# Kernel optimization log

Measured on AMD Instinct MI355X. Metric: run time of the kernel, lower is better.

## Reference

```python
import jax, jax.numpy as jnp
import numpy as np

FP8_MAX = 448.0  # finfo(float8_e4m3fn).max
G = 128          # quantization block size


def _fp8_roundtrip(x):
    # emulate storage/rounding in float8_e4m3fn
    return x.astype(jnp.float8_e4m3fn).astype(jnp.float32)


def _quant_dequant_act(x, g=G):
    """Dynamic per-token, per-128-column-group fp8 quantization, then dequant.
    Matches fp8_act_quant: scale = amax(group)/FP8_MAX, q = clip(x/scale)."""
    lead, K = x.shape[:-1], x.shape[-1]
    xg = x.reshape(*lead, K // g, g)
    amax = jnp.max(jnp.abs(xg), axis=-1, keepdims=True)
    scale = jnp.maximum(amax, 1e-10) / FP8_MAX
    q = _fp8_roundtrip(jnp.clip(xg / scale, -FP8_MAX, FP8_MAX))
    return (q * scale).reshape(*lead, K)


def _dequant_weight(w, s, g=G):
    """Block-wise dequant: w [E,O,K] fp8 codes (stored as f32), s [E,O/g,K/g] scales."""
    E, O, K = w.shape
    wb = w.reshape(E, O // g, g, K // g, g)
    return (wb * s[:, :, None, :, None]).reshape(E, O, K)


def setup_inputs() -> dict:
    key = jax.random.key(0)
    ks = jax.random.split(key, 7)
    T, H, I, E, TK = 2048, 1024, 512, 16, 4
    hidden_states = jax.random.normal(ks[0], (T, H), dtype=jnp.float32)
    top_k_index = jax.random.randint(ks[1], (T, TK), 0, E)
    top_k_weights = jax.nn.softmax(jax.random.normal(ks[2], (T, TK), dtype=jnp.float32), axis=-1)
    # fp8-representable weight codes + positive block scale grids
    gate_up_proj = _fp8_roundtrip(jax.random.normal(ks[3], (E, 2 * I, H), dtype=jnp.float32) * 8.0)
    gate_up_proj_scale_inv = jax.random.uniform(ks[4], (E, (2 * I) // G, H // G), dtype=jnp.float32,
                                                minval=0.001, maxval=0.005)
    down_proj = _fp8_roundtrip(jax.random.normal(ks[5], (E, H, I), dtype=jnp.float32) * 8.0)
    down_proj_scale_inv = jax.random.uniform(ks[6], (E, H // G, I // G), dtype=jnp.float32,
                                             minval=0.001, maxval=0.005)
    return {
        "hidden_states": hidden_states,
        "top_k_index": top_k_index,
        "top_k_weights": top_k_weights,
        "gate_up_proj": gate_up_proj,
        "gate_up_proj_scale_inv": gate_up_proj_scale_inv,
        "down_proj": down_proj,
        "down_proj_scale_inv": down_proj_scale_inv,
    }


def reference(hidden_states, top_k_index, top_k_weights,
              gate_up_proj, gate_up_proj_scale_inv,
              down_proj, down_proj_scale_inv):
    E = gate_up_proj.shape[0]
    # dynamic activation quant (identical for every expert, since tokens are just gathered rows)
    x_deq = _quant_dequant_act(hidden_states)                       # [T, H]
    w_gu = _dequant_weight(gate_up_proj, gate_up_proj_scale_inv)    # [E, 2I, H]
    w_dn = _dequant_weight(down_proj, down_proj_scale_inv)          # [E, H, I]
    # gate_up GEMM for all experts; tokens not routed to e contribute with weight 0 below
    gate_up = jnp.einsum('th,eoh->teo', x_deq, w_gu)                # [T, E, 2I]
    gate, up = jnp.split(gate_up, 2, axis=-1)
    h = jax.nn.silu(gate) * up                                      # [T, E, I]
    h_deq = _quant_dequant_act(h)                                   # re-quantize intermediate
    expert_out = jnp.einsum('tei,ehi->teh', h_deq, w_dn)            # [T, E, H]
    # routing weight per (token, expert): sum of top_k weights whose index == e
    rw = jnp.einsum('tk,tke->te', top_k_weights,
                    jax.nn.one_hot(top_k_index, E, dtype=hidden_states.dtype))
    return jnp.einsum('teh,te->th', expert_out, rw)                 # [T, H] float32 accumulation
```

## Files before the change

### kernel.cpp

```cpp
#include <hip/hip_runtime.h>
#include <math.h>

#define T_TOK 2048
#define H_DIM 1024
#define I_DIM 512
#define N_EXP 16
#define TOPK  4
#define NPAIR (T_TOK*TOPK)

typedef unsigned short u16;
typedef unsigned char u8;
typedef __attribute__((ext_vector_type(4))) float f4v;

#define GLDS(g, l) __builtin_amdgcn_global_load_lds( \
    (const __attribute__((address_space(1))) void*)(g), \
    (__attribute__((address_space(3))) void*)(l), 16, 0, 0)

__device__ __forceinline__ float fp8_rt(float v) {
    float av = fabsf(v);
    if (av < 0.015625f) {
        return rintf(v * 512.0f) * 0.001953125f;
    }
    unsigned u = __float_as_uint(v);
    unsigned lsb = (u >> 20) & 1u;
    u = (u + 0x7FFFFu + lsb) & 0xFFF00000u;
    return __uint_as_float(u);
}

__device__ __forceinline__ unsigned f2fp8(float v) {
    unsigned u = __float_as_uint(v);
    unsigned s = (u >> 24) & 0x80u;
    float av = fabsf(v);
    if (av < 0.015625f) return s | (unsigned)(av * 512.0f);
    unsigned e = ((u >> 23) & 0xFFu) - 120u;
    return s | (e << 3) | ((u >> 20) & 7u);
}

__global__ void k_route2(const int* __restrict__ tki, int* __restrict__ counts,
                         int* __restrict__ lists) {
    __shared__ int cnt[16];
    int tid = threadIdx.x;
    if (tid < 16) cnt[tid] = 0;
    __syncthreads();
    #pragma unroll
    for (int j = 0; j < 8; ++j) {
        int p = tid * 8 + j;
        int e = tki[p];
        int pos = atomicAdd(&cnt[e], 1);
        lists[e * NPAIR + pos] = p;
    }
    __syncthreads();
    if (tid < 16) counts[tid] = cnt[tid];
}

#define NF4_GU (N_EXP * 2 * I_DIM * H_DIM / 4)
__global__ void k_prep(const float* __restrict__ wgu, u8* __restrict__ wgu_f8,
                       const float* __restrict__ wdn, u8* __restrict__ wdn_f8,
                       const float* __restrict__ x, u8* __restrict__ xq,
                       float* __restrict__ xs) {
    int bid = blockIdx.x, tid = threadIdx.x;
    if (bid < 24576) {
        int i = bid * 256 + tid;
        const float* in = wgu; u8* out = wgu_f8;
        if (i >= NF4_GU) { in = wdn; out = wdn_f8; i -= NF4_GU; }
        float4 a = ((const float4*)in)[i];
        unsigned pk = f2fp8(a.x) | (f2fp8(a.y) << 8) | (f2fp8(a.z) << 16) | (f2fp8(a.w) << 24);
        ((unsigned*)out)[i] = pk;
    } else {
        int t = bid - 24576;
        float4 v = ((const float4*)(x + (size_t)t * H_DIM))[tid];
        float a = fmaxf(fmaxf(fabsf(v.x), fabsf(v.y)), fmaxf(fabsf(v.z), fabsf(v.w)));
        #pragma unroll
        for (int m = 16; m >= 1; m >>= 1) a = fmaxf(a, __shfl_xor(a, m));
        float s = fmaxf(a, 1e-10f) / 448.0f;
        unsigned pk = f2fp8(fp8_rt(fminf(fmaxf(v.x / s, -448.f), 448.f)))
                    | (f2fp8(fp8_rt(fminf(fmaxf(v.y / s, -448.f), 448.f))) << 8)
                    | (f2fp8(fp8_rt(fminf(fmaxf(v.z / s, -448.f), 448.f))) << 16)
                    | (f2fp8(fp8_rt(fminf(fmaxf(v.w / s, -448.f), 448.f))) << 24);
        ((unsigned*)(xq + (size_t)t * H_DIM))[tid] = pk;
        if ((tid & 31) == 0) xs[t * 8 + (tid >> 5)] = s;
    }
}

__global__ __launch_bounds__(256, 3)
void k_gateup(const u8* __restrict__ xq, const float* __restrict__ xs,
              const int* __restrict__ counts, const int* __restrict__ lists,
              const u8* __restrict__ wgu, const float* __restrict__ sgu,
              const u8* __restrict__ zbuf, float* __restrict__ hbuf) {
    int bid = blockIdx.x;
    int e = bid & 15, tile = bid >> 4;
    int tt = tile >> 3, it = tile & 7;
    int n = counts[e];
    if (tt * 64 >= n) return;

    __shared__ __align__(16) u8 sm[2][24576];
    __shared__ float xs_l[64][8];
    __shared__ int ptok[64];

    int tid = threadIdx.x;
    int w = tid >> 6, lane = tid & 63;
    int m = w & 1, q = w >> 1;
    int l15 = lane & 15, l4 = lane >> 4;

    if (tid < 64) {
        int slot = tt * 64 + tid;
        ptok[tid] = (slot < n) ? lists[e * NPAIR + slot] : -1;
    }
    __syncthreads();
    {
        int r = tid >> 2, kb4 = (tid & 3) * 2;
        int p = ptok[r];
        xs_l[r][kb4]     = (p >= 0) ? xs[(p >> 2) * 8 + kb4]     : 0.f;
        xs_l[r][kb4 + 1] = (p >= 0) ? xs[(p >> 2) * 8 + kb4 + 1] : 0.f;
    }

    const u8* wbase = wgu + (size_t)e * (2 * I_DIM) * H_DIM;
    const u8* srcB[4];
    #pragma unroll
    for (int j = 0; j < 4; ++j) {
        int s = j * 256 + tid;
        int row = s >> 3, c8 = s & 7, cg = c8 ^ (row & 7);
        int nrow = (row < 64) ? it * 64 + row : 448 + it * 64 + row;
        srcB[j] = wbase + (size_t)nrow * H_DIM + cg * 16;
    }
    const u8* srcA[2];
    #pragma unroll
    for (int j = 0; j < 2; ++j) {
        int s = j * 256 + tid;
        int row = s >> 3, c8 = s & 7, cg = c8 ^ (row & 7);
        int p = ptok[row];
        srcA[j] = (p >= 0) ? xq + (size_t)(p >> 2) * H_DIM + cg * 16 : zbuf;
    }

    int idxA[2][4], idxB[4][4];
    #pragma unroll
    for (int fm = 0; fm < 2; ++fm) {
        int ar = m * 32 + fm * 16 + l15;
        #pragma unroll
        for (int kg = 0; kg < 4; ++kg) {
            int u = kg * 4 + l4;
            idxA[fm][kg] = 16384 + ar * 128 + (((u >> 1) ^ (ar & 7)) << 4) + ((u & 1) << 3);
        }
    }
    #pragma unroll
    for (int nf = 0; nf < 4; ++nf) {
        int br = q * 64 + nf * 16 + l15;
        #pragma unroll
        for (int kg = 0; kg < 4; ++kg) {
            int u = kg * 4 + l4;
            idxB[nf][kg] = br * 128 + (((u >> 1) ^ (br & 7)) << 4) + ((u & 1) << 3);
        }
    }

    auto stage = [&](int buf) {
        #pragma unroll
        for (int j = 0; j < 4; ++j) { GLDS(srcB[j], &sm[buf][(j * 256 + tid) * 16]); srcB[j] += 128; }
        #pragma unroll
        for (int j = 0; j < 2; ++j) { GLDS(srcA[j], &sm[buf][16384 + (j * 256 + tid) * 16]); srcA[j] += 128; }
    };

    f4v master[2][4], part[2][4];
    #pragma unroll
    for (int a = 0; a < 2; ++a)
        #pragma unroll
        for (int b = 0; b < 4; ++b) { master[a][b] = (f4v){0,0,0,0}; part[a][b] = (f4v){0,0,0,0}; }

    const float* swp = sgu + e * 64 + (q ? 4 + (it >> 1) : (it >> 1)) * 8;

    stage(0);
    __syncthreads();

    for (int t = 0; t < 8; ++t) {
        if (t < 7) stage((t + 1) & 1);
        const u8* buf = &sm[t & 1][0];
        #pragma unroll
        for (int kg = 0; kg < 4; ++kg) {
            long a0 = *(const long*)&buf[idxA[0][kg]];
            long a1 = *(const long*)&buf[idxA[1][kg]];
            #pragma unroll
            for (int nf = 0; nf < 4; ++nf) {
                long b = *(const long*)&buf[idxB[nf][kg]];
                part[0][nf] = __builtin_amdgcn_mfma_f32_16x16x32_fp8_fp8(a0, b, part[0][nf], 0, 0, 0);
                part[1][nf] = __builtin_amdgcn_mfma_f32_16x16x32_fp8_fp8(a1, b, part[1][nf], 0, 0, 0);
            }
        }
        {
            float sw = swp[t];
            #pragma unroll
            for (int fm = 0; fm < 2; ++fm) {
                float c0 = xs_l[m * 32 + fm * 16 + l4 * 4 + 0][t] * sw;
                float c1 = xs_l[m * 32 + fm * 16 + l4 * 4 + 1][t] * sw;
                float c2 = xs_l[m * 32 + fm * 16 + l4 * 4 + 2][t] * sw;
                float c3 = xs_l[m * 32 + fm * 16 + l4 * 4 + 3][t] * sw;
                #pragma unroll
                for (int nf = 0; nf < 4; ++nf) {
                    master[fm][nf][0] += c0 * part[fm][nf][0];
                    master[fm][nf][1] += c1 * part[fm][nf][1];
                    master[fm][nf][2] += c2 * part[fm][nf][2];
                    master[fm][nf][3] += c3 * part[fm][nf][3];
                    part[fm][nf] = (f4v){0,0,0,0};
                }
            }
        }
        __syncthreads();
    }

    float* Ul = (float*)sm;
    if (q == 1) {
        #pragma unroll
        for (int fm = 0; fm < 2; ++fm)
            #pragma unroll
            for (int nf = 0; nf < 4; ++nf)
                #pragma unroll
                for (int r = 0; r < 4; ++r)
                    Ul[(m * 32 + fm * 16 + l4 * 4 + r) * 65 + nf * 16 + l15] = master[fm][nf][r];
    }
    __syncthreads();
    if (q == 0) {
        #pragma unroll
        for (int fm = 0; fm < 2; ++fm)
            #pragma unroll
            for (int r = 0; r < 4; ++r) {
                int row = m * 32 + fm * 16 + l4 * 4 + r;
                int p = ptok[row];
                if (p < 0) continue;
                float* drow = hbuf + (size_t)p * I_DIM + it * 64;
                #pragma unroll
                for (int nf = 0; nf < 4; ++nf) {
                    float g = master[fm][nf][r];
                    float u = Ul[row * 65 + nf * 16 + l15];
                    drow[nf * 16 + l15] = (g / (1.0f + expf(-g))) * u;
                }
            }
    }
}

__global__ void k_quant_h(const float* __restrict__ h, u8* __restrict__ hq,
                          float* __restrict__ hs) {
    int p = blockIdx.x, tid = threadIdx.x;
    float4 v = ((const float4*)(h + (size_t)p * I_DIM))[tid];
    float a = fmaxf(fmaxf(fabsf(v.x), fabsf(v.y)), fmaxf(fabsf(v.z), fabsf(v.w)));
    #pragma unroll
    for (int m = 16; m >= 1; m >>= 1) a = fmaxf(a, __shfl_xor(a, m));
    float s = fmaxf(a, 1e-10f) / 448.0f;
    unsigned pk = f2fp8(fp8_rt(fminf(fmaxf(v.x / s, -448.f), 448.f)))
                | (f2fp8(fp8_rt(fminf(fmaxf(v.y / s, -448.f), 448.f))) << 8)
                | (f2fp8(fp8_rt(fminf(fmaxf(v.z / s, -448.f), 448.f))) << 16)
                | (f2fp8(fp8_rt(fminf(fmaxf(v.w / s, -448.f), 448.f))) << 24);
    ((unsigned*)(hq + (size_t)p * I_DIM))[tid] = pk;
    if ((tid & 31) == 0) hs[p * 4 + (tid >> 5)] = s;
}

__global__ __launch_bounds__(256, 3)
void k_down(const u8* __restrict__ hq, const float* __restrict__ hs,
            const int* __restrict__ counts, const int* __restrict__ lists,
            const u8* __restrict__ wdn, const float* __restrict__ sdn,
            const float* __restrict__ tkw, const u8* __restrict__ zbuf,
            float* __restrict__ dout) {
    int bid = blockIdx.x;
    int e = bid & 15, tile = bid >> 4;
    int tt = tile >> 3, nt = tile & 7;
    int n = counts[e];
    if (tt * 64 >= n) return;

    __shared__ __align__(16) u8 sm[2][24576];
    __shared__ float hs_l[64][4];
    __shared__ float rw_l[64];
    __shared__ int ptok[64];

    int tid = threadIdx.x;
    int w = tid >> 6, lane = tid & 63;
    int m = w & 1, q = w >> 1;
    int l15 = lane & 15, l4 = lane >> 4;

    if (tid < 64) {
        int slot = tt * 64 + tid;
        ptok[tid] = (slot < n) ? lists[e * NPAIR + slot] : -1;
    }
    __syncthreads();
    {
        int r = tid >> 2, kb = tid & 3;
        int p = ptok[r];
        hs_l[r][kb] = (p >= 0) ? hs[p * 4 + kb] : 0.f;
        if (tid < 64) rw_l[tid] = (ptok[tid] >= 0) ? tkw[ptok[tid]] : 0.f;
    }

    const u8* wbase = wdn + (size_t)e * H_DIM * I_DIM;
    const u8* srcB[4];
    #pragma unroll
    for (int j = 0; j < 4; ++j) {
        int s = j * 256 + tid;
        int row = s >> 3, c8 = s & 7, cg = c8 ^ (row & 7);
        srcB[j] = wbase + (size_t)(nt * 128 + row) * I_DIM + cg * 16;
    }
    const u8* srcA[2];
    #pragma unroll
    for (int j = 0; j < 2; ++j) {
        int s = j * 256 + tid;
        int row = s >> 3, c8 = s & 7, cg = c8 ^ (row & 7);
        int p = ptok[row];
        srcA[j] = (p >= 0) ? hq + (size_t)p * I_DIM + cg * 16 : zbuf;
    }

    int idxA[2][4], idxB[4][4];
    #pragma unroll
    for (int fm = 0; fm < 2; ++fm) {
        int ar = m * 32 + fm * 16 + l15;
        #pragma unroll
        for (int kg = 0; kg < 4; ++kg) {
            int u = kg * 4 + l4;
            idxA[fm][kg] = 16384 + ar * 128 + (((u >> 1) ^ (ar & 7)) << 4) + ((u & 1) << 3);
        }
    }
    #pragma unroll
    for (int nf = 0; nf < 4; ++nf) {
        int br = q * 64 + nf * 16 + l15;
        #pragma unroll
        for (int kg = 0; kg < 4; ++kg) {
            int u = kg * 4 + l4;
            idxB[nf][kg] = br * 128 + (((u >> 1) ^ (br & 7)) << 4) + ((u & 1) << 3);
        }
    }

    auto stage = [&](int buf) {
        #pragma unroll
        for (int j = 0; j < 4; ++j) { GLDS(srcB[j], &sm[buf][(j * 256 + tid) * 16]); srcB[j] += 128; }
        #pragma unroll
        for (int j = 0; j < 2; ++j) { GLDS(srcA[j], &sm[buf][16384 + (j * 256 + tid) * 16]); srcA[j] += 128; }
    };

    f4v master[2][4], part[2][4];
    #pragma unroll
    for (int a = 0; a < 2; ++a)
        #pragma unroll
        for (int b = 0; b < 4; ++b) { master[a][b] = (f4v){0,0,0,0}; part[a][b] = (f4v){0,0,0,0}; }

    const float* swp = sdn + (e * 8 + nt) * 4;

    stage(0);
    __syncthreads();

    for (int t = 0; t < 4; ++t) {
        if (t < 3) stage((t + 1) & 1);
        const u8* buf = &sm[t & 1][0];
        #pragma unroll
        for (int kg = 0; kg < 4; ++kg) {
            long a0 = *(const long*)&buf[idxA[0][kg]];
            long a1 = *(const long*)&buf[idxA[1][kg]];
            #pragma unroll
            for (int nf = 0; nf < 4; ++nf) {
                long b = *(const long*)&buf[idxB[nf][kg]];
                part[0][nf] = __builtin_amdgcn_mfma_f32_16x16x32_fp8_fp8(a0, b, part[0][nf], 0, 0, 0);
                part[1][nf] = __builtin_amdgcn_mfma_f32_16x16x32_fp8_fp8(a1, b, part[1][nf], 0, 0, 0);
            }
        }
        {
            float sw = swp[t];
            #pragma unroll
            for (int fm = 0; fm < 2; ++fm) {
                float c0 = hs_l[m * 32 + fm * 16 + l4 * 4 + 0][t] * sw;
                float c1 = hs_l[m * 32 + fm * 16 + l4 * 4 + 1][t] * sw;
                float c2 = hs_l[m * 32 + fm * 16 + l4 * 4 + 2][t] * sw;
                float c3 = hs_l[m * 32 + fm * 16 + l4 * 4 + 3][t] * sw;
                #pragma unroll
                for (int nf = 0; nf < 4; ++nf) {
                    master[fm][nf][0] += c0 * part[fm][nf][0];
                    master[fm][nf][1] += c1 * part[fm][nf][1];
                    master[fm][nf][2] += c2 * part[fm][nf][2];
                    master[fm][nf][3] += c3 * part[fm][nf][3];
                    part[fm][nf] = (f4v){0,0,0,0};
                }
            }
        }
        __syncthreads();
    }

    #pragma unroll
    for (int fm = 0; fm < 2; ++fm)
        #pragma unroll
        for (int r = 0; r < 4; ++r) {
            int row = m * 32 + fm * 16 + l4 * 4 + r;
            int p = ptok[row];
            if (p < 0) continue;
            float rw = rw_l[row];
            float* drow = dout + (size_t)p * H_DIM + nt * 128 + q * 64;
            #pragma unroll
            for (int nf = 0; nf < 4; ++nf)
                drow[nf * 16 + l15] = rw * master[fm][nf][r];
        }
}

__global__ void k_reduce(const float* __restrict__ dout, float* __restrict__ out) {
    int i = blockIdx.x * 256 + threadIdx.x;
    int t = i >> 8, h4 = i & 255;
    const float4* d = (const float4*)dout;
    float4 a = d[(size_t)(t * 4 + 0) * 256 + h4];
    float4 b = d[(size_t)(t * 4 + 1) * 256 + h4];
    float4 c = d[(size_t)(t * 4 + 2) * 256 + h4];
    float4 e = d[(size_t)(t * 4 + 3) * 256 + h4];
    float4 r;
    r.x = a.x + b.x + c.x + e.x;
    r.y = a.y + b.y + c.y + e.y;
    r.z = a.z + b.z + c.z + e.z;
    r.w = a.w + b.w + c.w + e.w;
    ((float4*)out)[i] = r;
}

extern "C" void kernel_launch(void* const* d_in, const int* in_sizes, int n_in,
                              void* d_out, int out_size, void* d_ws, size_t ws_size,
                              hipStream_t stream) {
    const float* hs_in = (const float*)d_in[0];
    const int*   tki = (const int*)d_in[1];
    const float* tkw = (const float*)d_in[2];
    const float* wgu = (const float*)d_in[3];
    const float* sgu = (const float*)d_in[4];
    const float* wdn = (const float*)d_in[5];
    const float* sdn = (const float*)d_in[6];
    float* out = (float*)d_out;

    char* ws = (char*)d_ws;
    const size_t MB = 1024 * 1024;
    u8*    wgu_f8 = (u8*)(ws);
    float* dout   = (float*)(ws);
    u8*    wdn_f8 = (u8*)(ws + 32 * MB);
    u8*    xq     = (u8*)(ws + 40 * MB);
    float* xs     = (float*)(ws + 42 * MB);
    float* hbuf   = (float*)(ws + 43 * MB);
    u8*    hq     = (u8*)(ws + 59 * MB);
    float* hs     = (float*)(ws + 63 * MB);
    int*   counts = (int*)(ws + 64 * MB);
    u8*    zbuf   = (u8*)(ws + 64 * MB + 4096);
    int*   lists  = (int*)(ws + 64 * MB + 65536);

    hipMemsetAsync(ws + 64 * MB, 0, 8192, stream);

    k_route2<<<1, 1024, 0, stream>>>(tki, counts, lists);
    k_prep<<<26624, 256, 0, stream>>>(wgu, wgu_f8, wdn, wdn_f8, hs_in, xq, xs);
    k_gateup<<<2048, 256, 0, stream>>>(xq, xs, counts, lists, wgu_f8, sgu, zbuf, hbuf);
    k_quant_h<<<NPAIR, 128, 0, stream>>>(hbuf, hq, hs);
    k_down<<<2048, 256, 0, stream>>>(hq, hs, counts, lists, wdn_f8, sdn, tkw, zbuf, dout);
    k_reduce<<<T_TOK * H_DIM / 1024, 256, 0, stream>>>(dout, out);
}
```

Baseline: 214.1 us.

## Fuse routing and zero-fill into prep kernel with grid-stride weight conversion

Moves the expert routing (count/list build) and the zero-buffer clear into an extra block of the prep kernel. This removes a memset and a separate single-block launch. The weight fp8 conversion now uses 3328 blocks that each handle up to 8 float4 elements in a strided loop, instead of one element per thread across 24576 blocks, which cuts block scheduling overhead. The risk is that the single routing block now does 32 iterations with 256 threads and may sit on the critical path of the launch. The zbuf clear also covers only 4096 bytes, whereas the old memset cleared counts as well; counts is now written directly, so this stays consistent.

```diff
diff --git a/kernel.cpp b/kernel.cpp
--- a/kernel.cpp
+++ b/kernel.cpp
@@ -36,38 +36,30 @@
     return s | (e << 3) | ((u >> 20) & 7u);
 }
 
-__global__ void k_route2(const int* __restrict__ tki, int* __restrict__ counts,
-                         int* __restrict__ lists) {
-    __shared__ int cnt[16];
-    int tid = threadIdx.x;
-    if (tid < 16) cnt[tid] = 0;
-    __syncthreads();
-    #pragma unroll
-    for (int j = 0; j < 8; ++j) {
-        int p = tid * 8 + j;
-        int e = tki[p];
-        int pos = atomicAdd(&cnt[e], 1);
-        lists[e * NPAIR + pos] = p;
-    }
-    __syncthreads();
-    if (tid < 16) counts[tid] = cnt[tid];
-}
-
-#define NF4_GU (N_EXP * 2 * I_DIM * H_DIM / 4)
+#define NF4_ALL 6291456
+#define NF4_GU  4194304
+#define CVT_STRIDE (3328 * 256)
 __global__ void k_prep(const float* __restrict__ wgu, u8* __restrict__ wgu_f8,
                        const float* __restrict__ wdn, u8* __restrict__ wdn_f8,
                        const float* __restrict__ x, u8* __restrict__ xq,
-                       float* __restrict__ xs) {
+                       float* __restrict__ xs, const int* __restrict__ tki,
+                       int* __restrict__ counts, int* __restrict__ lists,
+                       u8* __restrict__ zbuf) {
     int bid = blockIdx.x, tid = threadIdx.x;
-    if (bid < 24576) {
-        int i = bid * 256 + tid;
-        const float* in = wgu; u8* out = wgu_f8;
-        if (i >= NF4_GU) { in = wdn; out = wdn_f8; i -= NF4_GU; }
-        float4 a = ((const float4*)in)[i];
-        unsigned pk = f2fp8(a.x) | (f2fp8(a.y) << 8) | (f2fp8(a.z) << 16) | (f2fp8(a.w) << 24);
-        ((unsigned*)out)[i] = pk;
-    } else {
-        int t = bid - 24576;
+    if (bid < 3328) {
+        int base = bid * 256 + tid;
+        #pragma unroll
+        for (int j = 0; j < 8; ++j) {
+            int i = j * CVT_STRIDE + base;
+            if (i >= NF4_ALL) break;
+            const float* in = wgu; u8* out = wgu_f8; int k = i;
+            if (k >= NF4_GU) { in = wdn; out = wdn_f8; k -= NF4_GU; }
+            float4 a = ((const float4*)in)[k];
+            unsigned pk = f2fp8(a.x) | (f2fp8(a.y) << 8) | (f2fp8(a.z) << 16) | (f2fp8(a.w) << 24);
+            ((unsigned*)out)[k] = pk;
+        }
+    } else if (bid < 5376) {
+        int t = bid - 3328;
         float4 v = ((const float4*)(x + (size_t)t * H_DIM))[tid];
         float a = fmaxf(fmaxf(fabsf(v.x), fabsf(v.y)), fmaxf(fabsf(v.z), fabsf(v.w)));
         #pragma unroll
@@ -79,6 +71,20 @@
                     | (f2fp8(fp8_rt(fminf(fmaxf(v.w / s, -448.f), 448.f))) << 24);
         ((unsigned*)(xq + (size_t)t * H_DIM))[tid] = pk;
         if ((tid & 31) == 0) xs[t * 8 + (tid >> 5)] = s;
+    } else {
+        __shared__ int cnt[16];
+        if (tid < 16) cnt[tid] = 0;
+        ((int4*)zbuf)[tid] = (int4){0, 0, 0, 0};
+        __syncthreads();
+        #pragma unroll 4
+        for (int j = 0; j < 32; ++j) {
+            int p = j * 256 + tid;
+            int e = tki[p];
+            int pos = atomicAdd(&cnt[e], 1);
+            lists[e * NPAIR + pos] = p;
+        }
+        __syncthreads();
+        if (tid < 16) counts[tid] = cnt[tid];
     }
 }
 
@@ -432,10 +438,8 @@
     u8*    zbuf   = (u8*)(ws + 64 * MB + 4096);
     int*   lists  = (int*)(ws + 64 * MB + 65536);
 
-    hipMemsetAsync(ws + 64 * MB, 0, 8192, stream);
-
-    k_route2<<<1, 1024, 0, stream>>>(tki, counts, lists);
-    k_prep<<<26624, 256, 0, stream>>>(wgu, wgu_f8, wdn, wdn_f8, hs_in, xq, xs);
+    k_prep<<<5377, 256, 0, stream>>>(wgu, wgu_f8, wdn, wdn_f8, hs_in, xq, xs,
+                                     tki, counts, lists, zbuf);
     k_gateup<<<2048, 256, 0, stream>>>(xq, xs, counts, lists, wgu_f8, sgu, zbuf, hbuf);
     k_quant_h<<<NPAIR, 128, 0, stream>>>(hbuf, hq, hs);
     k_down<<<2048, 256, 0, stream>>>(hq, hs, counts, lists, wdn_f8, sdn, tkw, zbuf, dout);
```

Result: no change. 217.0 us (+1.4%).
